# Performance work log

Hardware: AMD Instinct MI355X
Metric: run time of the kernel (lower is better)

Reference implementation:

```python
import jax, jax.numpy as jnp
import numpy as np

K = 16  # number of neighbors (init kwarg k)
N_POINTS = 8_000_000
D_FEAT = 6


def setup_inputs() -> dict:
    key = jax.random.key(0)
    k1, k2, k3 = jax.random.split(key, 3)
    P = jax.random.normal(k1, (N_POINTS, D_FEAT), dtype=jnp.float32)
    W = jax.random.normal(k2, (3, 10), dtype=jnp.float32) * 0.1  # nn.Linear(10, 3) weight
    b = jax.random.normal(k3, (3,), dtype=jnp.float32) * 0.1     # nn.Linear(10, 3) bias
    i = 12345
    return {"P": P, "W": W, "b": b, "i": i}


def reference(P, W, b, i):
    # --- knn(i): note torch .topk defaults to largest=True, so this faithfully
    # selects the K points with the LARGEST distance to point i.
    pi = P[i, :3]                                   # [3]
    d = jnp.linalg.norm(P[:, :3] - pi, axis=1)      # [N] streaming distance pass
    _, idx = jax.lax.top_k(d, K)                    # [K]
    near = P[idx]                                   # [K, D]
    nloc = near[:, :3]                              # [K, 3]

    # --- rel_pos_enc, vectorized over all K neighbors (one tiny GEMM)
    diff = pi[None, :] - nloc                       # [K, 3]
    dist = jnp.linalg.norm(diff, axis=1, keepdims=True)  # [K, 1]
    feat = jnp.concatenate(
        [jnp.broadcast_to(pi, (K, 3)), nloc, diff, dist], axis=1
    )                                               # [K, 10]
    R = feat @ W.T + b                              # [K, 3]

    # --- forward: concat neighbor coords with encoding
    return jnp.concatenate([nloc, R], axis=1)       # [K, 6]
```

## Files before the change

### kernel.cpp

```cpp
#include <hip/hip_runtime.h>
#include <math.h>

#define KTOP 16
#define B1   504
#define T1   512
#define NC   (B1 * KTOP)
#define T2   512

typedef unsigned long long ull;

__device__ __forceinline__ ull pack_key(float d, unsigned idx) {
    return ((ull)__float_as_uint(d) << 32) | (ull)(0xFFFFFFFFu - idx);
}

__device__ __forceinline__ void insert_key(ull (&k)[KTOP], ull key) {
    ull t = key;
#pragma unroll
    for (int j = 0; j < KTOP; ++j) {
        const ull a = k[j];
        const bool c = (t > a);
        k[j] = c ? t : a;
        t    = c ? a : t;
    }
}

__device__ __forceinline__ float dist3(float x, float y, float z,
                                       float px, float py, float pz) {
#pragma clang fp contract(off)
    const float dx = x - px;
    const float dy = y - py;
    const float dz = z - pz;
    const float s  = (dx * dx + dy * dy) + dz * dz;
    return sqrtf(s);
}

__global__ __launch_bounds__(T1, 1) void pass1_topk(const float* __restrict__ P,
                                                    const int*   __restrict__ ipq,
                                                    int n,
                                                    ull* __restrict__ cand) {
    const int tid    = threadIdx.x;
    const int gid    = blockIdx.x * T1 + tid;
    const int stride = B1 * T1;

    const int i0 = ipq[0];
    const float pix = P[6 * i0 + 0];
    const float piy = P[6 * i0 + 1];
    const float piz = P[6 * i0 + 2];

    ull k[KTOP];
#pragma unroll
    for (int j = 0; j < KTOP; ++j) k[j] = 0ull;

    const float4* __restrict__ P4 = (const float4*)P;
    const int nPairs = n >> 1;

    for (int pp = gid; pp < nPairs; pp += stride) {
        const float4 q0 = P4[3 * pp + 0];
        const float4 q1 = P4[3 * pp + 1];
        const float4 q2 = P4[3 * pp + 2];
        const float dA = dist3(q0.x, q0.y, q0.z, pix, piy, piz);
        const float dB = dist3(q1.z, q1.w, q2.x, pix, piy, piz);
        const ull keyA = pack_key(dA, (unsigned)(2 * pp));
        const ull keyB = pack_key(dB, (unsigned)(2 * pp + 1));
        if (keyA > k[KTOP - 1]) insert_key(k, keyA);
        if (keyB > k[KTOP - 1]) insert_key(k, keyB);
    }
    if ((n & 1) && gid == 0) {
        const int p = n - 1;
        const float d = dist3(P[6 * p], P[6 * p + 1], P[6 * p + 2], pix, piy, piz);
        const ull key = pack_key(d, (unsigned)p);
        if (key > k[KTOP - 1]) insert_key(k, key);
    }

    __shared__ ull s_w[T1 / 64];
    __shared__ ull s_best;
    const int lane = tid & 63;
    const int wid  = tid >> 6;

    for (int r = 0; r < KTOP; ++r) {
        const ull mk = k[0];
        ull rv = mk;
#pragma unroll
        for (int m = 32; m >= 1; m >>= 1) {
            const ull ov = __shfl_xor(rv, m);
            if (ov > rv) rv = ov;
        }
        if (lane == 0) s_w[wid] = rv;
        __syncthreads();
        if (tid == 0) {
            ull b = s_w[0];
            for (int w = 1; w < T1 / 64; ++w) if (s_w[w] > b) b = s_w[w];
            s_best = b;
            cand[blockIdx.x * KTOP + r] = b;
        }
        __syncthreads();
        if (mk == s_best) {
#pragma unroll
            for (int j = 0; j < KTOP - 1; ++j) k[j] = k[j + 1];
            k[KTOP - 1] = 0ull;
        }
    }
}

__global__ __launch_bounds__(T2, 1) void pass2_final(const float* __restrict__ P,
                                                     const int*   __restrict__ ipq,
                                                     const float* __restrict__ W,
                                                     const float* __restrict__ bvec,
                                                     const ull*   __restrict__ cand,
                                                     float* __restrict__ out) {
    __shared__ ull keys[NC];
    __shared__ ull s_w[T2 / 64];
    __shared__ ull s_best;
    __shared__ ull s_final[KTOP];

    const int tid  = threadIdx.x;
    const int lane = tid & 63;
    const int wid  = tid >> 6;

    ull mk = 0ull; int ms = -1;
#pragma unroll
    for (int j = 0; j < 16; ++j) {
        const int s = tid + j * T2;
        if (s < NC) {
            const ull v = cand[s];
            keys[s] = v;
            if (v > mk) { mk = v; ms = s; }
        }
    }
    __syncthreads();

    for (int r = 0; r < KTOP; ++r) {
        ull rv = mk;
#pragma unroll
        for (int m = 32; m >= 1; m >>= 1) {
            const ull ov = __shfl_xor(rv, m);
            if (ov > rv) rv = ov;
        }
        if (lane == 0) s_w[wid] = rv;
        __syncthreads();
        if (tid == 0) {
            ull b = s_w[0];
            for (int w = 1; w < T2 / 64; ++w) if (s_w[w] > b) b = s_w[w];
            s_best = b;
            s_final[r] = b;
        }
        __syncthreads();
        const ull best = s_best;
        if (mk == best) {
            keys[ms] = 0ull;
            mk = 0ull; ms = -1;
#pragma unroll
            for (int j = 0; j < 16; ++j) {
                const int s = tid + j * T2;
                if (s < NC) {
                    const ull v = keys[s];
                    if (v > mk) { mk = v; ms = s; }
                }
            }
        }
    }
    __syncthreads();

    if (tid < KTOP) {
        const ull kk = s_final[tid];
        const float d = __uint_as_float((unsigned)(kk >> 32));
        const unsigned idx = 0xFFFFFFFFu - (unsigned)(kk & 0xFFFFFFFFull);
        const int   i0  = ipq[0];
        const float pix = P[6 * i0 + 0], piy = P[6 * i0 + 1], piz = P[6 * i0 + 2];
        const float nx  = P[6 * (size_t)idx + 0];
        const float ny  = P[6 * (size_t)idx + 1];
        const float nz  = P[6 * (size_t)idx + 2];
        float dx, dy, dz;
        {
#pragma clang fp contract(off)
            dx = pix - nx; dy = piy - ny; dz = piz - nz;
        }
        const float feat[10] = { pix, piy, piz, nx, ny, nz, dx, dy, dz, d };
        float R[3];
#pragma unroll
        for (int r = 0; r < 3; ++r) {
            float acc = bvec[r];
#pragma unroll
            for (int c = 0; c < 10; ++c) acc += feat[c] * W[r * 10 + c];
            R[r] = acc;
        }
        out[6 * tid + 0] = nx;   out[6 * tid + 1] = ny;   out[6 * tid + 2] = nz;
        out[6 * tid + 3] = R[0]; out[6 * tid + 4] = R[1]; out[6 * tid + 5] = R[2];
    }
}

extern "C" void kernel_launch(void* const* d_in, const int* in_sizes, int n_in,
                              void* d_out, int out_size, void* d_ws, size_t ws_size,
                              hipStream_t stream) {
    const float* P    = (const float*)d_in[0];
    const float* W    = (const float*)d_in[1];
    const float* bvec = (const float*)d_in[2];
    const int*   ipq  = (const int*)d_in[3];
    float*       out  = (float*)d_out;

    const int n = in_sizes[0] / 6;
    ull* cand = (ull*)d_ws;

    pass1_topk<<<B1, T1, 0, stream>>>(P, ipq, n, cand);
    pass2_final<<<1, T2, 0, stream>>>(P, ipq, W, bvec, cand, out);
}
```

Measured before the change: 291.1 us.

## Process four points per iteration and merge sorted per-block lists in pass2

Pass1 now loads six float4s per iteration and handles four points at a time instead of two. Launch bounds change to allow four blocks per CU, and the grid grows to 512 blocks so it matches the 512 threads of pass2. Pass2 then has each thread read one block's already-sorted top-16 list into registers and pop from its head, instead of staging all candidates in shared memory and rescanning them. This trades some register pressure for more memory-level parallelism and a cheaper final merge. It relies on B1 being equal to T2.

```diff
diff --git a/kernel.cpp b/kernel.cpp
--- a/kernel.cpp
+++ b/kernel.cpp
@@ -2,9 +2,8 @@
 #include <math.h>
 
 #define KTOP 16
-#define B1   504
+#define B1   512
 #define T1   512
-#define NC   (B1 * KTOP)
 #define T2   512
 
 typedef unsigned long long ull;
@@ -34,7 +33,7 @@
     return sqrtf(s);
 }
 
-__global__ __launch_bounds__(T1, 1) void pass1_topk(const float* __restrict__ P,
+__global__ __launch_bounds__(T1, 4) void pass1_topk(const float* __restrict__ P,
                                                     const int*   __restrict__ ipq,
                                                     int n,
                                                     ull* __restrict__ cand) {
@@ -52,21 +51,29 @@
     for (int j = 0; j < KTOP; ++j) k[j] = 0ull;
 
     const float4* __restrict__ P4 = (const float4*)P;
-    const int nPairs = n >> 1;
+    const int nQuad = n >> 2;
 
-    for (int pp = gid; pp < nPairs; pp += stride) {
-        const float4 q0 = P4[3 * pp + 0];
-        const float4 q1 = P4[3 * pp + 1];
-        const float4 q2 = P4[3 * pp + 2];
-        const float dA = dist3(q0.x, q0.y, q0.z, pix, piy, piz);
-        const float dB = dist3(q1.z, q1.w, q2.x, pix, piy, piz);
-        const ull keyA = pack_key(dA, (unsigned)(2 * pp));
-        const ull keyB = pack_key(dB, (unsigned)(2 * pp + 1));
-        if (keyA > k[KTOP - 1]) insert_key(k, keyA);
-        if (keyB > k[KTOP - 1]) insert_key(k, keyB);
+    for (int q = gid; q < nQuad; q += stride) {
+        const float4 r0 = P4[6 * q + 0];
+        const float4 r1 = P4[6 * q + 1];
+        const float4 r2 = P4[6 * q + 2];
+        const float4 r3 = P4[6 * q + 3];
+        const float4 r4 = P4[6 * q + 4];
+        const float4 r5 = P4[6 * q + 5];
+        const float d0 = dist3(r0.x, r0.y, r0.z, pix, piy, piz);
+        const float d1 = dist3(r1.z, r1.w, r2.x, pix, piy, piz);
+        const float d2 = dist3(r3.x, r3.y, r3.z, pix, piy, piz);
+        const float d3 = dist3(r4.z, r4.w, r5.x, pix, piy, piz);
+        const ull k0 = pack_key(d0, (unsigned)(4 * q + 0));
+        const ull k1 = pack_key(d1, (unsigned)(4 * q + 1));
+        const ull k2 = pack_key(d2, (unsigned)(4 * q + 2));
+        const ull k3 = pack_key(d3, (unsigned)(4 * q + 3));
+        if (k0 > k[KTOP - 1]) insert_key(k, k0);
+        if (k1 > k[KTOP - 1]) insert_key(k, k1);
+        if (k2 > k[KTOP - 1]) insert_key(k, k2);
+        if (k3 > k[KTOP - 1]) insert_key(k, k3);
     }
-    if ((n & 1) && gid == 0) {
-        const int p = n - 1;
+    for (int p = (nQuad << 2) + gid; p < n; p += stride) {
         const float d = dist3(P[6 * p], P[6 * p + 1], P[6 * p + 2], pix, piy, piz);
         const ull key = pack_key(d, (unsigned)p);
         if (key > k[KTOP - 1]) insert_key(k, key);
@@ -108,7 +115,6 @@
                                                      const float* __restrict__ bvec,
                                                      const ull*   __restrict__ cand,
                                                      float* __restrict__ out) {
-    __shared__ ull keys[NC];
     __shared__ ull s_w[T2 / 64];
     __shared__ ull s_best;
     __shared__ ull s_final[KTOP];
@@ -117,19 +123,13 @@
     const int lane = tid & 63;
     const int wid  = tid >> 6;
 
-    ull mk = 0ull; int ms = -1;
+    ull k[KTOP];
+    const ull* __restrict__ my = cand + (size_t)tid * KTOP;
 #pragma unroll
-    for (int j = 0; j < 16; ++j) {
-        const int s = tid + j * T2;
-        if (s < NC) {
-            const ull v = cand[s];
-            keys[s] = v;
-            if (v > mk) { mk = v; ms = s; }
-        }
-    }
-    __syncthreads();
+    for (int j = 0; j < KTOP; ++j) k[j] = my[j];
 
     for (int r = 0; r < KTOP; ++r) {
+        const ull mk = k[0];
         ull rv = mk;
 #pragma unroll
         for (int m = 32; m >= 1; m >>= 1) {
@@ -145,18 +145,10 @@
             s_final[r] = b;
         }
         __syncthreads();
-        const ull best = s_best;
-        if (mk == best) {
-            keys[ms] = 0ull;
-            mk = 0ull; ms = -1;
+        if (mk == s_best) {
 #pragma unroll
-            for (int j = 0; j < 16; ++j) {
-                const int s = tid + j * T2;
-                if (s < NC) {
-                    const ull v = keys[s];
-                    if (v > mk) { mk = v; ms = s; }
-                }
-            }
+            for (int j = 0; j < KTOP - 1; ++j) k[j] = k[j + 1];
+            k[KTOP - 1] = 0ull;
         }
     }
     __syncthreads();
```

Measured after the change: 291.7 us (median of 2 runs). Within noise of the previous version (+0.2%).
